# Optimization experiments

Hardware: AMD Instinct MI355X
Metric: run time of the kernel (lower is better)

The kernel has to match this reference:

```python
import jax, jax.numpy as jnp
import numpy as np

EPS = 1e-12  # torch F.normalize default eps


def setup_inputs() -> dict:
    key = jax.random.key(0)
    k1, k2, k3 = jax.random.split(key, 3)
    b, c, H, W = 16, 384, 48, 48
    heads = 8
    x = jax.random.normal(k1, (b, c, H, W), dtype=jnp.float32)
    # torch Linear weight init scale ~ 1/sqrt(fan_in); use scaled normals
    w_qkv = jax.random.normal(k2, (c, 3 * c), dtype=jnp.float32) / np.sqrt(c)
    temperature = jnp.ones((1, heads, 1, 1), dtype=jnp.float32)
    w_out = jax.random.normal(k3, (c, c), dtype=jnp.float32) / np.sqrt(c)
    b_out = jnp.zeros((c,), dtype=jnp.float32)
    return {"x": x, "w_qkv": w_qkv, "temperature": temperature,
            "w_out": w_out, "b_out": b_out}


def reference(x, w_qkv, temperature, w_out, b_out):
    b, c, H, W = x.shape
    h = temperature.shape[1]
    d = c // h
    n = H * W
    # b c h w -> b n c
    xt = x.reshape(b, c, n).transpose(0, 2, 1)
    qkv = xt @ w_qkv  # [b, n, 3c]
    q, k, v = jnp.split(qkv, 3, axis=-1)
    q = q.reshape(b, n, h, d).transpose(0, 2, 1, 3)  # b h n d
    k = k.reshape(b, n, h, d).transpose(0, 2, 3, 1)  # b h d n
    v = v.reshape(b, n, h, d).transpose(0, 2, 1, 3)  # b h n d
    # L2 normalize over the token axis (n): q over dim=-2, k over dim=-1
    q = q / jnp.maximum(jnp.sqrt(jnp.sum(q * q, axis=-2, keepdims=True)), EPS)
    k = k / jnp.maximum(jnp.sqrt(jnp.sum(k * k, axis=-1, keepdims=True)), EPS)
    k = k * temperature
    # cross-covariance attention over channels: [b, h, d, d]
    attn = jnp.einsum('bhpn,bhnq->bhpq', k, q)
    attn = jax.nn.softmax(attn, axis=-1)
    out = jnp.einsum('bhnp,bhpq->bhnq', v, attn)  # [b, h, n, d]
    out = out.transpose(0, 2, 1, 3).reshape(b, n, c)  # b n (h d)
    out = out @ w_out + b_out
    # b n c -> b c h w
    out = out.transpose(0, 2, 1).reshape(b, c, H, W)
    return out
```

## Files before the change

### kernel.cpp

```cpp
#include <hip/hip_runtime.h>
#include <cstdint>

typedef __attribute__((ext_vector_type(8))) short short8;
typedef __attribute__((ext_vector_type(4))) float f32x4;
typedef unsigned int u32;
typedef unsigned short u16;

#define NTOK 2304
#define CDIM 384

__device__ __forceinline__ u16 f2bf(float f) {
    u32 u = __builtin_bit_cast(u32, f);
    u32 r = (u + 0x7FFFu + ((u >> 16) & 1u)) >> 16;
    return (u16)r;
}
__device__ __forceinline__ float bf2f(u32 h) {
    u32 u = h << 16;
    return __builtin_bit_cast(float, u);
}

__global__ __launch_bounds__(256) void transpose_all(
    const float* __restrict__ x, const float* __restrict__ w_qkv,
    const float* __restrict__ w_out,
    u16* __restrict__ xT, u16* __restrict__ xbf,
    u16* __restrict__ wqkvT, u16* __restrict__ wv, u16* __restrict__ woutT)
{
    __shared__ float tile[64][65];
    const int bz = blockIdx.z;
    const float* src; int Csz; char* dT; char* dC = nullptr;
    int dcCol0 = 0; long dcRowB = 0;
    if (bz < 16) {
        src = x + (long)bz * 384 * 2304; Csz = 2304;
        dT = (char*)(xT + (long)bz * 2304 * 384);
        dC = (char*)(xbf + (long)bz * 384 * 2304);
        dcCol0 = 0; dcRowB = 2304 * 2;
    } else if (bz == 16) {
        if (blockIdx.x >= 18) return;
        src = w_qkv; Csz = 1152;
        dT = (char*)wqkvT; dC = (char*)wv; dcCol0 = 768; dcRowB = 768;
    } else {
        if (blockIdx.x >= 6) return;
        src = w_out; Csz = 384;
        dT = (char*)woutT;
    }
    const int c0 = blockIdx.x * 64;
    const int k0 = blockIdx.y * 64;
    const int t = threadIdx.x;
    const int rr = t >> 2, cc4 = (t & 3) * 16;

    const float* srow = src + (long)(k0 + rr) * Csz + c0 + cc4;
#pragma unroll
    for (int i = 0; i < 4; ++i) {
        float4 v = *(const float4*)(srow + i * 4);
        tile[rr][cc4 + i*4 + 0] = v.x;
        tile[rr][cc4 + i*4 + 1] = v.y;
        tile[rr][cc4 + i*4 + 2] = v.z;
        tile[rr][cc4 + i*4 + 3] = v.w;
    }
    __syncthreads();

    {
        char* drow = dT + (long)(c0 + rr) * (CDIM * 2);
        const int sw = (rr & 7) << 4;
#pragma unroll
        for (int half = 0; half < 2; ++half) {
            u32 pk[4];
#pragma unroll
            for (int i = 0; i < 4; ++i) {
                float v0 = tile[cc4 + half*8 + 2*i][rr];
                float v1 = tile[cc4 + half*8 + 2*i + 1][rr];
                pk[i] = (u32)f2bf(v0) | ((u32)f2bf(v1) << 16);
            }
            uint4 q; q.x = pk[0]; q.y = pk[1]; q.z = pk[2]; q.w = pk[3];
            const int inrow = (k0 + cc4 + half*8) * 2;
            *(uint4*)(drow + (inrow ^ sw)) = q;
        }
    }
    if (dC && c0 >= dcCol0) {
        char* drow = dC + (long)(k0 + rr) * dcRowB;
        const int sw = (rr & 7) << 4;
#pragma unroll
        for (int half = 0; half < 2; ++half) {
            u32 pk[4];
#pragma unroll
            for (int i = 0; i < 4; ++i) {
                float v0 = tile[rr][cc4 + half*8 + 2*i];
                float v1 = tile[rr][cc4 + half*8 + 2*i + 1];
                pk[i] = (u32)f2bf(v0) | ((u32)f2bf(v1) << 16);
            }
            uint4 q; q.x = pk[0]; q.y = pk[1]; q.z = pk[2]; q.w = pk[3];
            const int inrow = (c0 - dcCol0 + cc4 + half*8) * 2;
            *(uint4*)(drow + (inrow ^ sw)) = q;
        }
    }
}

template<int MODE, int KT, int GX, int GY>
__global__ __launch_bounds__(256) void mfma_gemm(
    const u16* __restrict__ A, long aBatch,
    const u16* __restrict__ Bm, long bBatch,
    void* __restrict__ Ovoid, long oBatch, int ostride,
    const float* __restrict__ bias)
{
    constexpr int KB  = KT * 128;
    constexpr int KE  = KT * 64;
    constexpr int NWG = GX * GY * 16;
    __shared__ __attribute__((aligned(16))) u16 As[2][128 * 64];
    __shared__ __attribute__((aligned(16))) u16 Bs[2][128 * 64];

    const int lid = blockIdx.x + GX * (blockIdx.y + GY * blockIdx.z);
    const int swzid = (lid & 7) * (NWG / 8) + (lid >> 3);
    const int b   = swzid / (GX * GY);
    const int rem = swzid % (GX * GY);
    const int m0 = (rem % GX) * 128, n0 = (rem / GX) * 128;

    const u16* Ab = A + (long)b * aBatch + (long)m0 * KE;
    const u16* Bb = Bm + (long)b * bBatch + (long)n0 * KE;
    const int t = threadIdx.x;
    const int w = t >> 6, l = t & 63;
    const int wm = (w >> 1) * 64, wn = (w & 1) * 64;
    const int srow = t >> 3;
    const int scol = (t & 7) * 16;
    f32x4 acc[4][4] = {};

    auto stage = [&](int buf, int kt) {
        const int kbyte = kt * 128;
#pragma unroll
        for (int i = 0; i < 4; ++i) {
            const int row = srow + i * 32;
            const long so = (long)row * KB + kbyte + scol;
            const int d = (i * 256 + t) * 16;
            __builtin_amdgcn_global_load_lds(
                (const __attribute__((address_space(1))) u32*)((const char*)Ab + so),
                (__attribute__((address_space(3))) u32*)((char*)&As[buf][0] + d), 16, 0, 0);
            __builtin_amdgcn_global_load_lds(
                (const __attribute__((address_space(1))) u32*)((const char*)Bb + so),
                (__attribute__((address_space(3))) u32*)((char*)&Bs[buf][0] + d), 16, 0, 0);
        }
    };

    stage(0, 0);
    __syncthreads();
    int cur = 0;
#pragma unroll 1
    for (int kt = 0; kt < KT; ++kt) {
        if (kt < KT - 1) stage(cur ^ 1, kt + 1);
        const char* Ac = (const char*)&As[cur][0];
        const char* Bc = (const char*)&Bs[cur][0];
#pragma unroll
        for (int kk = 0; kk < 2; ++kk) {
            short8 af[4], bfr[4];
#pragma unroll
            for (int mi = 0; mi < 4; ++mi) {
                const int m = wm + mi * 16 + (l & 15);
                const int off = m * 128 + ((kk * 64 + (l >> 4) * 16) ^ ((m & 7) << 4));
                af[mi] = *(const short8*)(Ac + off);
            }
#pragma unroll
            for (int ni = 0; ni < 4; ++ni) {
                const int n = wn + ni * 16 + (l & 15);
                const int off = n * 128 + ((kk * 64 + (l >> 4) * 16) ^ ((n & 7) << 4));
                bfr[ni] = *(const short8*)(Bc + off);
            }
#pragma unroll
            for (int mi = 0; mi < 4; ++mi)
#pragma unroll
                for (int ni = 0; ni < 4; ++ni)
                    acc[mi][ni] = __builtin_amdgcn_mfma_f32_16x16x32_bf16(
                        af[mi], bfr[ni], acc[mi][ni], 0, 0, 0);
        }
        __syncthreads();
        cur ^= 1;
    }

    if (MODE == 0) {
        u16* O = (u16*)Ovoid + (long)b * oBatch;
#pragma unroll
        for (int mi = 0; mi < 4; ++mi) {
            const int mb = m0 + wm + mi * 16 + (l >> 4) * 4;
#pragma unroll
            for (int ni = 0; ni < 4; ++ni) {
                const int n = n0 + wn + ni * 16 + (l & 15);
#pragma unroll
                for (int r = 0; r < 4; ++r)
                    O[(long)(mb + r) * ostride + n] = f2bf(acc[mi][ni][r]);
            }
        }
    } else if (MODE == 1) {
        float* O = (float*)Ovoid + (long)b * oBatch;
#pragma unroll
        for (int mi = 0; mi < 4; ++mi) {
            const int mb = m0 + wm + mi * 16 + (l >> 4) * 4;
#pragma unroll
            for (int r = 0; r < 4; ++r) {
                const float bb = bias[mb + r];
#pragma unroll
                for (int ni = 0; ni < 4; ++ni) {
                    const int n = n0 + wn + ni * 16 + (l & 15);
                    O[(long)(mb + r) * ostride + n] = acc[mi][ni][r] + bb;
                }
            }
        }
    } else {
        char* Ob = (char*)Ovoid + (long)b * oBatch * 2;
#pragma unroll
        for (int mi = 0; mi < 4; ++mi) {
            const int mb = m0 + wm + mi * 16 + (l >> 4) * 4;
#pragma unroll
            for (int ni = 0; ni < 4; ++ni) {
                const int n = n0 + wn + ni * 16 + (l & 15);
#pragma unroll
                for (int r = 0; r < 4; ++r) {
                    const int m = mb + r;
                    const long byteoff = (long)m * (ostride * 2) +
                        (((long)n * 2) ^ ((m & 7) << 4));
                    *(u16*)(Ob + byteoff) = f2bf(acc[mi][ni][r]);
                }
            }
        }
    }
}

__global__ __launch_bounds__(256) void sm_fold(
    const u16* __restrict__ Tp,
    const u16* __restrict__ wT,
    const float* __restrict__ temp,
    const u16* __restrict__ woutT,
    u16* __restrict__ W2T)
{
    __shared__ float Sp[4][48][48];
    __shared__ float S[48][49];
    __shared__ float invk[48], invq[48];
    __shared__ __attribute__((aligned(16))) u16 Sbf[48 * 64];
    const int h = blockIdx.x, b = blockIdx.y, t = threadIdx.x;
    const int w = t >> 6, l = t & 63, lr = l & 15, lk = (l >> 4) * 8;
    const int h48 = h * 48;

    const u16* Tk = Tp + ((long)b * 768 + 384 + h48) * CDIM;
    {
        f32x4 acc[3][3] = {};
#pragma unroll
        for (int ks = 0; ks < 3; ++ks) {
            const int k0 = w * 96 + ks * 32 + lk;
            short8 af[3], bfr[3];
#pragma unroll
            for (int mi = 0; mi < 3; ++mi)
                af[mi] = *(const short8*)(Tk + (long)(mi * 16 + lr) * CDIM + k0);
#pragma unroll
            for (int ni = 0; ni < 3; ++ni) {
                const int row = h48 + ni * 16 + lr;
                const char* base = (const char*)wT + (long)row * 768;
                bfr[ni] = *(const short8*)(base + ((k0 * 2) ^ ((row & 7) << 4)));
            }
#pragma unroll
            for (int mi = 0; mi < 3; ++mi)
#pragma unroll
                for (int ni = 0; ni < 3; ++ni)
                    acc[mi][ni] = __builtin_amdgcn_mfma_f32_16x16x32_bf16(
                        af[mi], bfr[ni], acc[mi][ni], 0, 0, 0);
        }
#pragma unroll
        for (int mi = 0; mi < 3; ++mi)
#pragma unroll
            for (int ni = 0; ni < 3; ++ni)
#pragma unroll
                for (int r = 0; r < 4; ++r)
                    Sp[w][mi * 16 + (l >> 4) * 4 + r][ni * 16 + lr] = acc[mi][ni][r];
    }
    if (t < 96) {
        const int ch = (t < 48) ? (h48 + t) : (384 + h48 + (t - 48));
        const u16* trow = Tp + ((long)b * 768 + ch) * CDIM;
        const char* wrow = (const char*)wT + (long)ch * 768;
        const int sw = (ch & 7) << 4;
        float s = 0.f;
#pragma unroll 4
        for (int i = 0; i < 48; ++i) {
            short8 tv = *(const short8*)(trow + i * 8);
            short8 wv = *(const short8*)(wrow + ((i * 16) ^ sw));
#pragma unroll
            for (int e = 0; e < 8; ++e)
                s += bf2f((u16)tv[e]) * bf2f((u16)wv[e]);
        }
        float inv = 1.0f / fmaxf(sqrtf(fmaxf(s, 0.f)), 1e-12f);
        if (t < 48) invq[t] = inv; else invk[t - 48] = inv;
    }
    __syncthreads();
    for (int idx = t; idx < 2304; idx += 256) {
        const int p = idx / 48, q = idx % 48;
        S[p][q] = Sp[0][p][q] + Sp[1][p][q] + Sp[2][p][q] + Sp[3][p][q];
    }
    __syncthreads();
    if (t < 48) {
        const float sc = temp[h] * invk[t];
        float row[48];
        float mx = -1e30f;
#pragma unroll 8
        for (int q = 0; q < 48; ++q) {
            row[q] = S[t][q] * sc * invq[q];
            mx = fmaxf(mx, row[q]);
        }
        float ssum = 0.f;
#pragma unroll 8
        for (int q = 0; q < 48; ++q) {
            row[q] = __expf(row[q] - mx);
            ssum += row[q];
        }
        float inv = 1.0f / ssum;
        const int sw = (t & 7) << 4;
#pragma unroll
        for (int g = 0; g < 8; ++g) {
            u32 pk[4];
#pragma unroll
            for (int e = 0; e < 4; ++e) {
                const int q0 = g * 8 + 2 * e;
                float v0 = (q0 < 48) ? row[q0] * inv : 0.f;
                float v1 = (q0 + 1 < 48) ? row[q0 + 1] * inv : 0.f;
                pk[e] = (u32)f2bf(v0) | ((u32)f2bf(v1) << 16);
            }
            uint4 qv; qv.x = pk[0]; qv.y = pk[1]; qv.z = pk[2]; qv.w = pk[3];
            *(uint4*)((char*)Sbf + t * 128 + ((g * 16) ^ sw)) = qv;
        }
    }
    __syncthreads();
    {
        const char* SbfB = (const char*)Sbf;
        const int jw = w * 96;
        f32x4 fac[3][6] = {};
#pragma unroll
        for (int ks = 0; ks < 2; ++ks) {
            const int ka = ks * 64 + (l >> 4) * 16;
            const int kb = h * 96 + ka;
            short8 af[3], bfr[6];
#pragma unroll
            for (int mi = 0; mi < 3; ++mi) {
                const int p = mi * 16 + lr;
                af[mi] = *(const short8*)(SbfB + p * 128 + (ka ^ ((p & 7) << 4)));
            }
#pragma unroll
            for (int ni = 0; ni < 6; ++ni) {
                const int j = jw + ni * 16 + lr;
                bfr[ni] = *(const short8*)((const char*)woutT + (long)j * 768 +
                                           (kb ^ ((j & 7) << 4)));
            }
#pragma unroll
            for (int mi = 0; mi < 3; ++mi)
#pragma unroll
                for (int ni = 0; ni < 6; ++ni)
                    fac[mi][ni] = __builtin_amdgcn_mfma_f32_16x16x32_bf16(
                        af[mi], bfr[ni], fac[mi][ni], 0, 0, 0);
        }
        char* Wb = (char*)W2T + (long)b * 294912;
#pragma unroll
        for (int mi = 0; mi < 3; ++mi)
#pragma unroll
            for (int ni = 0; ni < 6; ++ni)
#pragma unroll
                for (int r = 0; r < 4; ++r) {
                    const int p = mi * 16 + (l >> 4) * 4 + r;
                    const int j = jw + ni * 16 + lr;
                    const long byteoff = (long)j * 768 +
                        (((h48 + p) * 2) ^ ((j & 7) << 4));
                    *(u16*)(Wb + byteoff) = f2bf(fac[mi][ni][r]);
                }
    }
}

extern "C" void kernel_launch(void* const* d_in, const int* in_sizes, int n_in,
                              void* d_out, int out_size, void* d_ws, size_t ws_size,
                              hipStream_t stream) {
    const float* x     = (const float*)d_in[0];
    const float* w_qkv = (const float*)d_in[1];
    const float* temp  = (const float*)d_in[2];
    const float* w_out = (const float*)d_in[3];
    const float* b_out = (const float*)d_in[4];
    float* out = (float*)d_out;

    char* ws = (char*)d_ws;
    const size_t SZ_XBF = 16UL * 384 * 2304 * 2;
    const size_t SZ_XT  = 16UL * 2304 * 384 * 2;
    const size_t SZ_WQT = 1152UL * 384 * 2;
    const size_t SZ_WV  = 384UL * 384 * 2;
    const size_t SZ_WOT = 384UL * 384 * 2 + 256;
    const size_t SZ_G   = 16UL * 384 * 384 * 2;
    const size_t SZ_TP  = 16UL * 768 * 384 * 2;
    const size_t SZ_W2  = 16UL * 384 * 384 * 2;

    size_t off = 0;
    u16* xbf   = (u16*)(ws + off); off += SZ_XBF;
    u16* xT    = (u16*)(ws + off); off += SZ_XT;
    u16* wqkvT = (u16*)(ws + off); off += SZ_WQT;
    u16* wv    = (u16*)(ws + off); off += SZ_WV;
    u16* woutT = (u16*)(ws + off); off += SZ_WOT;
    u16* Gs    = (u16*)(ws + off); off += SZ_G;
    u16* Tp    = (u16*)(ws + off); off += SZ_TP;
    u16* W2T   = (u16*)(ws + off); off += SZ_W2;
    u16* W3    = (u16*)(ws + off);

    transpose_all<<<dim3(36, 6, 18), 256, 0, stream>>>(
        x, w_qkv, w_out, xT, xbf, wqkvT, wv, woutT);
    mfma_gemm<2, 36, 3, 3><<<dim3(3, 3, 16), 256, 0, stream>>>(
        xbf, 384L * 2304, xbf, 384L * 2304, Gs, 384L * 384, 384, nullptr);
    mfma_gemm<0, 6, 6, 3><<<dim3(6, 3, 16), 256, 0, stream>>>(
        wqkvT, 0L, Gs, 384L * 384, Tp, 768L * 384, 384, nullptr);
    sm_fold<<<dim3(8, 16), 256, 0, stream>>>(Tp, wqkvT, temp, woutT, W2T);
    mfma_gemm<2, 6, 3, 3><<<dim3(3, 3, 16), 256, 0, stream>>>(
        W2T, 384L * 384, wv, 0L, W3, 384L * 384, 384, nullptr);
    mfma_gemm<1, 6, 3, 18><<<dim3(3, 18, 16), 256, 0, stream>>>(
        W3, 384L * 384, xT, 384L * 2304, out, 384L * 2304, 2304, b_out);
}
```

Before: 124.0 us.

## Fuse middle GEMMs and softmax fold into one cooperative persistent kernel

Replaces four separate launches (Gram GEMM, Tp GEMM, softmax fold, W3 GEMM) with a single cooperative kernel of 256 blocks that runs the stages in sequence, separated by grid-wide syncs. The GEMM core and the fold logic are moved into device functions that work on a shared 64 KB LDS buffer. The goal is to remove the launch gaps and tail effects between these small kernels. In exchange it adds grid-sync cost, leaves many blocks idle in each stage, and keeps the old multi-kernel path as a fallback if the cooperative launch fails.

```diff
diff --git a/kernel.cpp b/kernel.cpp
--- a/kernel.cpp
+++ b/kernel.cpp
@@ -1,5 +1,8 @@
 #include <hip/hip_runtime.h>
+#include <hip/hip_cooperative_groups.h>
 #include <cstdint>
+
+namespace cg = cooperative_groups;
 
 typedef __attribute__((ext_vector_type(8))) short short8;
 typedef __attribute__((ext_vector_type(4))) float f32x4;
@@ -95,27 +98,13 @@
     }
 }
 
-template<int MODE, int KT, int GX, int GY>
-__global__ __launch_bounds__(256) void mfma_gemm(
-    const u16* __restrict__ A, long aBatch,
-    const u16* __restrict__ Bm, long bBatch,
-    void* __restrict__ Ovoid, long oBatch, int ostride,
-    const float* __restrict__ bias)
+template<int MODE, int KT>
+__device__ __forceinline__ void gemm_core(
+    const u16* __restrict__ Ab, const u16* __restrict__ Bb,
+    char* __restrict__ Obase, int m0, int n0, int ostride,
+    const float* __restrict__ bias, u16* As, u16* Bs)
 {
-    constexpr int KB  = KT * 128;
-    constexpr int KE  = KT * 64;
-    constexpr int NWG = GX * GY * 16;
-    __shared__ __attribute__((aligned(16))) u16 As[2][128 * 64];
-    __shared__ __attribute__((aligned(16))) u16 Bs[2][128 * 64];
-
-    const int lid = blockIdx.x + GX * (blockIdx.y + GY * blockIdx.z);
-    const int swzid = (lid & 7) * (NWG / 8) + (lid >> 3);
-    const int b   = swzid / (GX * GY);
-    const int rem = swzid % (GX * GY);
-    const int m0 = (rem % GX) * 128, n0 = (rem / GX) * 128;
-
-    const u16* Ab = A + (long)b * aBatch + (long)m0 * KE;
-    const u16* Bb = Bm + (long)b * bBatch + (long)n0 * KE;
+    constexpr int KB = KT * 128;
     const int t = threadIdx.x;
     const int w = t >> 6, l = t & 63;
     const int wm = (w >> 1) * 64, wn = (w & 1) * 64;
@@ -129,13 +118,13 @@
         for (int i = 0; i < 4; ++i) {
             const int row = srow + i * 32;
             const long so = (long)row * KB + kbyte + scol;
-            const int d = (i * 256 + t) * 16;
+            const int d = buf * 16384 + (i * 256 + t) * 16;
             __builtin_amdgcn_global_load_lds(
                 (const __attribute__((address_space(1))) u32*)((const char*)Ab + so),
-                (__attribute__((address_space(3))) u32*)((char*)&As[buf][0] + d), 16, 0, 0);
+                (__attribute__((address_space(3))) u32*)((char*)As + d), 16, 0, 0);
             __builtin_amdgcn_global_load_lds(
                 (const __attribute__((address_space(1))) u32*)((const char*)Bb + so),
-                (__attribute__((address_space(3))) u32*)((char*)&Bs[buf][0] + d), 16, 0, 0);
+                (__attribute__((address_space(3))) u32*)((char*)Bs + d), 16, 0, 0);
         }
     };
 
@@ -145,8 +134,8 @@
 #pragma unroll 1
     for (int kt = 0; kt < KT; ++kt) {
         if (kt < KT - 1) stage(cur ^ 1, kt + 1);
-        const char* Ac = (const char*)&As[cur][0];
-        const char* Bc = (const char*)&Bs[cur][0];
+        const char* Ac = (const char*)As + cur * 16384;
+        const char* Bc = (const char*)Bs + cur * 16384;
 #pragma unroll
         for (int kk = 0; kk < 2; ++kk) {
             short8 af[4], bfr[4];
@@ -174,7 +163,7 @@
     }
 
     if (MODE == 0) {
-        u16* O = (u16*)Ovoid + (long)b * oBatch;
+        u16* O = (u16*)Obase;
 #pragma unroll
         for (int mi = 0; mi < 4; ++mi) {
             const int mb = m0 + wm + mi * 16 + (l >> 4) * 4;
@@ -187,7 +176,7 @@
             }
         }
     } else if (MODE == 1) {
-        float* O = (float*)Ovoid + (long)b * oBatch;
+        float* O = (float*)Obase;
 #pragma unroll
         for (int mi = 0; mi < 4; ++mi) {
             const int mb = m0 + wm + mi * 16 + (l >> 4) * 4;
@@ -202,7 +191,6 @@
             }
         }
     } else {
-        char* Ob = (char*)Ovoid + (long)b * oBatch * 2;
 #pragma unroll
         for (int mi = 0; mi < 4; ++mi) {
             const int mb = m0 + wm + mi * 16 + (l >> 4) * 4;
@@ -214,25 +202,25 @@
                     const int m = mb + r;
                     const long byteoff = (long)m * (ostride * 2) +
                         (((long)n * 2) ^ ((m & 7) << 4));
-                    *(u16*)(Ob + byteoff) = f2bf(acc[mi][ni][r]);
+                    *(u16*)(Obase + byteoff) = f2bf(acc[mi][ni][r]);
                 }
             }
         }
     }
 }
 
-__global__ __launch_bounds__(256) void sm_fold(
-    const u16* __restrict__ Tp,
-    const u16* __restrict__ wT,
-    const float* __restrict__ temp,
-    const u16* __restrict__ woutT,
-    u16* __restrict__ W2T)
+__device__ __forceinline__ void sm_fold_core(
+    const u16* __restrict__ Tp, const u16* __restrict__ wT,
+    const float* __restrict__ temp, const u16* __restrict__ woutT,
+    u16* __restrict__ W2T, int h, int b, char* shb)
 {
-    __shared__ float Sp[4][48][48];
-    __shared__ float S[48][49];
-    __shared__ float invk[48], invq[48];
-    __shared__ __attribute__((aligned(16))) u16 Sbf[48 * 64];
-    const int h = blockIdx.x, b = blockIdx.y, t = threadIdx.x;
+    float* Sp  = (float*)shb;
+    float* S   = (float*)(shb + 36864);
+    float* invk = (float*)(shb + 46272);
+    float* invq = (float*)(shb + 46464);
+    u16* Sbf = (u16*)(shb + 46656);
+
+    const int t = threadIdx.x;
     const int w = t >> 6, l = t & 63, lr = l & 15, lk = (l >> 4) * 8;
     const int h48 = h * 48;
 
@@ -265,7 +253,8 @@
             for (int ni = 0; ni < 3; ++ni)
 #pragma unroll
                 for (int r = 0; r < 4; ++r)
-                    Sp[w][mi * 16 + (l >> 4) * 4 + r][ni * 16 + lr] = acc[mi][ni][r];
+                    Sp[w * 2304 + (mi * 16 + (l >> 4) * 4 + r) * 48 + ni * 16 + lr]
+                        = acc[mi][ni][r];
     }
     if (t < 96) {
         const int ch = (t < 48) ? (h48 + t) : (384 + h48 + (t - 48));
@@ -287,7 +276,7 @@
     __syncthreads();
     for (int idx = t; idx < 2304; idx += 256) {
         const int p = idx / 48, q = idx % 48;
-        S[p][q] = Sp[0][p][q] + Sp[1][p][q] + Sp[2][p][q] + Sp[3][p][q];
+        S[p * 49 + q] = Sp[idx] + Sp[2304 + idx] + Sp[4608 + idx] + Sp[6912 + idx];
     }
     __syncthreads();
     if (t < 48) {
@@ -296,7 +285,7 @@
         float mx = -1e30f;
 #pragma unroll 8
         for (int q = 0; q < 48; ++q) {
-            row[q] = S[t][q] * sc * invq[q];
+            row[q] = S[t * 49 + q] * sc * invq[q];
             mx = fmaxf(mx, row[q]);
         }
         float ssum = 0.f;
@@ -363,6 +352,94 @@
                     *(u16*)(Wb + byteoff) = f2bf(fac[mi][ni][r]);
                 }
     }
+}
+
+__global__ __launch_bounds__(256, 2) void mid_fused(
+    const u16* __restrict__ xbf, const u16* __restrict__ wqkvT,
+    const u16* __restrict__ wv, const u16* __restrict__ woutT,
+    const float* __restrict__ temp,
+    u16* __restrict__ Gs, u16* __restrict__ Tp,
+    u16* __restrict__ W2T, u16* __restrict__ W3)
+{
+    __shared__ __attribute__((aligned(16))) char shb[65536];
+    u16* As = (u16*)shb;
+    u16* Bs = (u16*)(shb + 32768);
+    cg::grid_group grid = cg::this_grid();
+    const int bid = blockIdx.x;
+
+    if (bid < 144) {
+        const int swzid = (bid & 7) * 18 + (bid >> 3);
+        const int b = swzid / 9, rem = swzid % 9;
+        const int m0 = (rem % 3) * 128, n0 = (rem / 3) * 128;
+        const u16* xb = xbf + (long)b * 384 * NTOK;
+        gemm_core<2, 36>(xb + (long)m0 * NTOK, xb + (long)n0 * NTOK,
+                         (char*)Gs + (long)b * 294912, m0, n0, 384,
+                         nullptr, As, Bs);
+    }
+    __threadfence();
+    grid.sync();
+
+    for (int tile = bid; tile < 288; tile += 256) {
+        const int swzid = (tile & 7) * 36 + (tile >> 3);
+        const int b = swzid / 18, rem = swzid % 18;
+        const int m0 = (rem % 6) * 128, n0 = (rem / 6) * 128;
+        gemm_core<0, 6>(wqkvT + (long)m0 * 384,
+                        Gs + (long)b * 147456 + (long)n0 * 384,
+                        (char*)Tp + (long)b * 589824, m0, n0, 384,
+                        nullptr, As, Bs);
+    }
+    __threadfence();
+    grid.sync();
+
+    if (bid < 128) {
+        sm_fold_core(Tp, wqkvT, temp, woutT, W2T, bid & 7, bid >> 3, shb);
+    }
+    __threadfence();
+    grid.sync();
+
+    if (bid < 144) {
+        const int swzid = (bid & 7) * 18 + (bid >> 3);
+        const int b = swzid / 9, rem = swzid % 9;
+        const int m0 = (rem % 3) * 128, n0 = (rem / 3) * 128;
+        gemm_core<2, 6>(W2T + (long)b * 147456 + (long)m0 * 384,
+                        wv + (long)n0 * 384,
+                        (char*)W3 + (long)b * 294912, m0, n0, 384,
+                        nullptr, As, Bs);
+    }
+}
+
+template<int MODE, int KT, int GX, int GY>
+__global__ __launch_bounds__(256) void mfma_gemm(
+    const u16* __restrict__ A, long aBatch,
+    const u16* __restrict__ Bm, long bBatch,
+    void* __restrict__ Ovoid, long oBatch, int ostride,
+    const float* __restrict__ bias)
+{
+    constexpr int KE  = KT * 64;
+    constexpr int NWG = GX * GY * 16;
+    __shared__ __attribute__((aligned(16))) u16 As[2][128 * 64];
+    __shared__ __attribute__((aligned(16))) u16 Bs[2][128 * 64];
+
+    const int lid = blockIdx.x + GX * (blockIdx.y + GY * blockIdx.z);
+    const int swzid = (lid & 7) * (NWG / 8) + (lid >> 3);
+    const int b   = swzid / (GX * GY);
+    const int rem = swzid % (GX * GY);
+    const int m0 = (rem % GX) * 128, n0 = (rem / GX) * 128;
+
+    char* Obase = (char*)Ovoid + (long)b * oBatch * (MODE == 1 ? 4 : 2);
+    gemm_core<MODE, KT>(A + (long)b * aBatch + (long)m0 * KE,
+                        Bm + (long)b * bBatch + (long)n0 * KE,
+                        Obase, m0, n0, ostride, bias,
+                        &As[0][0], &Bs[0][0]);
+}
+
+__global__ __launch_bounds__(256) void sm_fold_kernel(
+    const u16* __restrict__ Tp, const u16* __restrict__ wT,
+    const float* __restrict__ temp, const u16* __restrict__ woutT,
+    u16* __restrict__ W2T)
+{
+    __shared__ __attribute__((aligned(16))) char shb[52800];
+    sm_fold_core(Tp, wT, temp, woutT, W2T, blockIdx.x, blockIdx.y, shb);
 }
 
 extern "C" void kernel_launch(void* const* d_in, const int* in_sizes, int n_in,
@@ -398,13 +475,27 @@
 
     transpose_all<<<dim3(36, 6, 18), 256, 0, stream>>>(
         x, w_qkv, w_out, xT, xbf, wqkvT, wv, woutT);
-    mfma_gemm<2, 36, 3, 3><<<dim3(3, 3, 16), 256, 0, stream>>>(
-        xbf, 384L * 2304, xbf, 384L * 2304, Gs, 384L * 384, 384, nullptr);
-    mfma_gemm<0, 6, 6, 3><<<dim3(6, 3, 16), 256, 0, stream>>>(
-        wqkvT, 0L, Gs, 384L * 384, Tp, 768L * 384, 384, nullptr);
-    sm_fold<<<dim3(8, 16), 256, 0, stream>>>(Tp, wqkvT, temp, woutT, W2T);
-    mfma_gemm<2, 6, 3, 3><<<dim3(3, 3, 16), 256, 0, stream>>>(
-        W2T, 384L * 384, wv, 0L, W3, 384L * 384, 384, nullptr);
+
+    {
+        void* margs[] = {
+            (void*)&xbf, (void*)&wqkvT, (void*)&wv, (void*)&woutT,
+            (void*)&temp, (void*)&Gs, (void*)&Tp, (void*)&W2T, (void*)&W3
+        };
+        hipError_t cerr = hipLaunchCooperativeKernel(
+            reinterpret_cast<void*>(mid_fused),
+            dim3(256, 1, 1), dim3(256, 1, 1), margs, 0, stream);
+        if (cerr != hipSuccess) {
+            mfma_gemm<2, 36, 3, 3><<<dim3(3, 3, 16), 256, 0, stream>>>(
+                xbf, 384L * 2304, xbf, 384L * 2304, Gs, 384L * 384, 384, nullptr);
+            mfma_gemm<0, 6, 6, 3><<<dim3(6, 3, 16), 256, 0, stream>>>(
+                wqkvT, 0L, Gs, 384L * 384, Tp, 768L * 384, 384, nullptr);
+            sm_fold_kernel<<<dim3(8, 16), 256, 0, stream>>>(
+                Tp, wqkvT, temp, woutT, W2T);
+            mfma_gemm<2, 6, 3, 3><<<dim3(3, 3, 16), 256, 0, stream>>>(
+                W2T, 384L * 384, wv, 0L, W3, 384L * 384, 384, nullptr);
+        }
+    }
+
     mfma_gemm<1, 6, 3, 18><<<dim3(3, 18, 16), 256, 0, stream>>>(
         W3, 384L * 384, xT, 384L * 2304, out, 384L * 2304, 2304, b_out);
 }
```

Result: slower. 307.8 us (+148.2%).
